# Kernel optimization log

Hardware: AMD Instinct MI355X
Metric: run time of the kernel (lower is better)

## Reference

```python
import jax, jax.numpy as jnp
import numpy as np

H = 12      # attention heads
BS = 64     # BigBird block size
NEG = -1e9  # additive mask value


def setup_inputs() -> dict:
    key = jax.random.key(0)
    ks = jax.random.split(key, 12)
    L, B, S, D, C = 13, 2, 512, 768, 16
    nb = (B * S) // BS  # 16 blocks
    w = lambda k, shp: jax.random.normal(k, shp, jnp.float32) * 0.02
    return {
        "hidden_states": jax.random.normal(ks[0], (L, B, S, D), jnp.float32),
        "attention_mask": jnp.ones((B, S), jnp.int32),
        # 3 random key-blocks per middle query block, drawn from non-global blocks
        "rand_blocks": jax.random.randint(ks[1], (nb - 2, 3), 1, nb - 1, jnp.int32),
        "Wq": w(ks[2], (D, D)), "bq": jnp.zeros((D,), jnp.float32),
        "Wk": w(ks[3], (D, D)), "bk": jnp.zeros((D,), jnp.float32),
        "Wv": w(ks[4], (D, D)), "bv": jnp.zeros((D,), jnp.float32),
        "Wo": w(ks[5], (D, D)), "bo": jnp.zeros((D,), jnp.float32),
        "Wd": w(ks[6], (D, D)), "bd": jnp.zeros((D,), jnp.float32),
        "ln_g": jnp.ones((D,), jnp.float32), "ln_b": jnp.zeros((D,), jnp.float32),
        "Wc": w(ks[7], (D, C)), "bc": jnp.zeros((C,), jnp.float32),
    }


def _forward(hidden_states, attention_mask, rand_blocks,
             Wq, bq, Wk, bk, Wv, bv, Wo, bo, Wd, bd, ln_g, ln_b, Wc, bc):
    L, B, S, D = hidden_states.shape
    T = B * S
    hd = D // H
    nb = T // BS
    scale = 1.0 / np.sqrt(hd).astype(np.float32)

    # tensor_split + cat glue == reshape to one row per layer
    h = hidden_states.reshape(L, T, D)           # [L,T,D]
    mask = attention_mask.reshape(T)             # [T]

    def proj(W, b):
        return (h @ W + b).reshape(L, T, H, hd).transpose(0, 2, 1, 3)  # [L,H,T,hd]

    q, k, v = proj(Wq, bq), proj(Wk, bk), proj(Wv, bv)
    qb = q.reshape(L, H, nb, BS, hd)
    kb = k.reshape(L, H, nb, BS, hd)
    vb = v.reshape(L, H, nb, BS, hd)
    maskb = mask.reshape(nb, BS)

    # ---- middle query blocks: global(first,last) + window(i-1,i,i+1) + 3 random ----
    nm = nb - 2
    mid = jnp.arange(1, nb - 1)
    glob = jnp.broadcast_to(jnp.array([0, nb - 1]), (nm, 2))
    win = jnp.stack([mid - 1, mid, mid + 1], axis=-1)          # [nm,3]
    idx = jnp.concatenate([glob, win, rand_blocks], axis=1)    # [nm,8]

    kg = kb[:, :, idx]                                         # [L,H,nm,8,BS,hd]
    vg = vb[:, :, idx].reshape(L, H, nm, 8 * BS, hd)
    mg = maskb[idx].reshape(nm, 8 * BS)                        # [nm,8*BS]

    qm = qb[:, :, 1:nb - 1]                                    # [L,H,nm,BS,hd]
    s = jnp.einsum('lhnqd,lhnkbd->lhnqkb', qm, kg).reshape(L, H, nm, BS, 8 * BS) * scale
    s = jnp.where(mg[None, None, :, None, :] > 0, s, NEG)
    a = jax.nn.softmax(s, axis=-1)
    ctx_mid = jnp.einsum('lhnqk,lhnkd->lhnqd', a, vg)          # [L,H,nm,BS,hd]

    # ---- global query blocks (first & last) attend to everything ----
    qg = qb[:, :, jnp.array([0, nb - 1])]                      # [L,H,2,BS,hd]
    sg = jnp.einsum('lhgqd,lhtd->lhgqt', qg, k) * scale
    sg = jnp.where(mask[None, None, None, None, :] > 0, sg, NEG)
    ag = jax.nn.softmax(sg, axis=-1)
    ctx_g = jnp.einsum('lhgqt,lhtd->lhgqd', ag, v)             # [L,H,2,BS,hd]

    ctx = jnp.concatenate([ctx_g[:, :, 0:1], ctx_mid, ctx_g[:, :, 1:2]], axis=2)
    ctx = ctx.transpose(0, 2, 3, 1, 4).reshape(L, T, D)        # [L,T,D]
    attn_out = ctx @ Wo + bo

    # BertSelfOutput: dense + LayerNorm (dropout = identity in eval)
    hs = attn_out @ Wd + bd
    mu = hs.mean(-1, keepdims=True)
    var = hs.var(-1, keepdims=True)
    hs = (hs - mu) / jnp.sqrt(var + 1e-12) * ln_g + ln_b

    out = hs[-1]                                               # last layer row, [T,D]
    batch_out = out.reshape(B, S, D)                           # un-flatten glue
    return batch_out @ Wc + bc                                 # [B,S,classes]


def reference(hidden_states, attention_mask, rand_blocks,
              Wq, bq, Wk, bk, Wv, bv, Wo, bo, Wd, bd, ln_g, ln_b, Wc, bc):
    return _forward(hidden_states, attention_mask, rand_blocks,
                    Wq, bq, Wk, bk, Wv, bv, Wo, bo, Wd, bd, ln_g, ln_b, Wc, bc)
```

## Files before the change

### kernel.cpp

```cpp
#include <hip/hip_runtime.h>
#include <hip/hip_bf16.h>
#include <math.h>

#define TT    1024
#define DD    768
#define NHEAD 12
#define HDIM  64
#define NBLK  16
#define NMID  14
#define NCOUT 16

typedef __attribute__((ext_vector_type(4))) float f32x4;
typedef __attribute__((ext_vector_type(8))) short bfrag;

#define MFMA(a, b, c) __builtin_amdgcn_mfma_f32_16x16x32_bf16(a, b, c, 0, 0, 0)

__device__ __forceinline__ bfrag ldg8(const ushort* p) { return *(const bfrag*)p; }
__device__ __forceinline__ ushort f2bf(float f) {
    __hip_bfloat16 h = __float2bfloat16(f);
    return *(ushort*)&h;
}

__global__ __launch_bounds__(256) void prep_k(
    const float* __restrict__ X,
    const float* __restrict__ Wq, const float* __restrict__ Wk,
    const float* __restrict__ Wv, const float* __restrict__ Wo,
    const float* __restrict__ Wd,
    ushort* __restrict__ xb,
    ushort* __restrict__ qT, ushort* __restrict__ kT, ushort* __restrict__ vT,
    ushort* __restrict__ oT, ushort* __restrict__ dT)
{
    __shared__ float t[32][33];
    int bx = blockIdx.x;
    if (bx < 768) {
        int i = bx * 256 + threadIdx.x;
        float4 f = ((const float4*)X)[i];
        ushort4 u;
        u.x = f2bf(f.x); u.y = f2bf(f.y); u.z = f2bf(f.z); u.w = f2bf(f.w);
        ((ushort4*)xb)[i] = u;
        return;
    }
    int bz = bx - 768;
    int z = bz / 576;
    int rem = bz % 576;
    int k0 = (rem / 24) * 32, n0 = (rem % 24) * 32;
    const float* W; ushort* O;
    if (z == 0)      { W = Wq; O = qT; }
    else if (z == 1) { W = Wk; O = kT; }
    else if (z == 2) { W = Wv; O = vT; }
    else if (z == 3) { W = Wo; O = oT; }
    else             { W = Wd; O = dT; }
    int tx = threadIdx.x & 31, ty = threadIdx.x >> 5;
    #pragma unroll
    for (int i = 0; i < 4; i++)
        t[ty + i * 8][tx] = W[(k0 + ty + i * 8) * DD + n0 + tx];
    __syncthreads();
    #pragma unroll
    for (int i = 0; i < 4; i++)
        O[(n0 + ty + i * 8) * DD + k0 + tx] = f2bf(t[tx][ty + i * 8]);
}

__global__ __launch_bounds__(256) void qkv_mfma_k(
    const ushort* __restrict__ xb,
    const ushort* __restrict__ wqT, const ushort* __restrict__ wkT,
    const ushort* __restrict__ wvT,
    const float* __restrict__ bq, const float* __restrict__ bk,
    const float* __restrict__ bv,
    ushort* __restrict__ qo, ushort* __restrict__ ko, ushort* __restrict__ vTo)
{
    int z = blockIdx.z;
    const ushort* BT = (z == 0) ? wqT : (z == 1) ? wkT : wvT;
    const float* bias = (z == 0) ? bq : (z == 1) ? bk : bv;

    __shared__ float mo[4][16][4][64];
    int lane = threadIdx.x & 63, w = threadIdx.x >> 6;
    int lr = lane & 15, lg = lane >> 4;
    int row0 = blockIdx.x * 64;
    int h = blockIdx.y;
    int col0 = h * 64;

    f32x4 acc[16];
    #pragma unroll
    for (int p = 0; p < 16; p++) acc[p] = (f32x4){0, 0, 0, 0};
    const ushort* ap = xb + (size_t)(row0 + lr) * DD + w * 192 + lg * 8;
    const ushort* bp = BT + (size_t)(col0 + lr) * DD + w * 192 + lg * 8;
    #pragma unroll
    for (int ks = 0; ks < 6; ks++) {
        bfrag a0 = ldg8(ap + ks * 32);
        bfrag a1 = ldg8(ap + (size_t)16 * DD + ks * 32);
        bfrag a2 = ldg8(ap + (size_t)32 * DD + ks * 32);
        bfrag a3 = ldg8(ap + (size_t)48 * DD + ks * 32);
        #pragma unroll
        for (int nt = 0; nt < 4; nt++) {
            bfrag b = ldg8(bp + (size_t)nt * 16 * DD + ks * 32);
            acc[nt]      = MFMA(a0, b, acc[nt]);
            acc[4 + nt]  = MFMA(a1, b, acc[4 + nt]);
            acc[8 + nt]  = MFMA(a2, b, acc[8 + nt]);
            acc[12 + nt] = MFMA(a3, b, acc[12 + nt]);
        }
    }
    #pragma unroll
    for (int p = 0; p < 16; p++)
        #pragma unroll
        for (int j = 0; j < 4; j++)
            mo[w][p][j][lane] = acc[p][j];
    __syncthreads();

    #pragma unroll
    for (int pi = 0; pi < 4; pi++) {
        int p = w + pi * 4;
        int m = p >> 2, nt = p & 3;
        #pragma unroll
        for (int j = 0; j < 4; j++) {
            float of = mo[0][p][j][lane] + mo[1][p][j][lane] +
                       mo[2][p][j][lane] + mo[3][p][j][lane];
            int r = row0 + m * 16 + lg * 4 + j;
            int cc = nt * 16 + lr;
            ushort u = f2bf(of + bias[col0 + cc]);
            if (z == 2)      vTo[(size_t)(h * 64 + cc) * TT + r] = u;
            else if (z == 0) qo[(size_t)(h * TT + r) * 64 + cc] = u;
            else             ko[(size_t)(h * TT + r) * 64 + cc] = u;
        }
    }
}

template <int OUTF32>
__global__ __launch_bounds__(256) void mm_mfma_k(
    const ushort* __restrict__ A, const ushort* __restrict__ BT,
    const float* __restrict__ bias, void* __restrict__ out)
{
    __shared__ float mo[4][8][4][64];
    int lane = threadIdx.x & 63, w = threadIdx.x >> 6;
    int lr = lane & 15, lg = lane >> 4;
    int row0 = blockIdx.x * 32;
    int col0 = blockIdx.y * 64;

    f32x4 acc[8];
    #pragma unroll
    for (int p = 0; p < 8; p++) acc[p] = (f32x4){0, 0, 0, 0};
    const ushort* a0p = A + (size_t)(row0 + lr) * DD + w * 192 + lg * 8;
    const ushort* a1p = a0p + (size_t)16 * DD;
    const ushort* bp  = BT + (size_t)(col0 + lr) * DD + w * 192 + lg * 8;
    #pragma unroll
    for (int ks = 0; ks < 6; ks++) {
        bfrag a0 = ldg8(a0p + ks * 32);
        bfrag a1 = ldg8(a1p + ks * 32);
        #pragma unroll
        for (int nt = 0; nt < 4; nt++) {
            bfrag b = ldg8(bp + (size_t)nt * 16 * DD + ks * 32);
            acc[nt]     = MFMA(a0, b, acc[nt]);
            acc[4 + nt] = MFMA(a1, b, acc[4 + nt]);
        }
    }
    #pragma unroll
    for (int p = 0; p < 8; p++)
        #pragma unroll
        for (int j = 0; j < 4; j++)
            mo[w][p][j][lane] = acc[p][j];
    __syncthreads();

    #pragma unroll
    for (int pi = 0; pi < 2; pi++) {
        int p = w + pi * 4;
        int m = p >> 2, nt = p & 3;
        #pragma unroll
        for (int j = 0; j < 4; j++) {
            float of = mo[0][p][j][lane] + mo[1][p][j][lane] +
                       mo[2][p][j][lane] + mo[3][p][j][lane];
            int r = row0 + m * 16 + lg * 4 + j;
            int c = col0 + nt * 16 + lr;
            float v = of + bias[c];
            if (OUTF32) ((float*)out)[(size_t)r * DD + c] = v;
            else        ((ushort*)out)[(size_t)r * DD + c] = f2bf(v);
        }
    }
}

__device__ __forceinline__ void attn_core2x2(
    const ushort* __restrict__ kbf, const ushort* __restrict__ vT,
    const int* __restrict__ mask, const int kblk[2], int h,
    bfrag aq0, bfrag aq1, bfrag aq2, bfrag aq3, ushort* __restrict__ Pw,
    f32x4 (&o0)[4], f32x4 (&o1)[4], float (&l0)[4], float (&l1)[4])
{
    int lane = threadIdx.x & 63, lr = lane & 15, lg = lane >> 4;
    #pragma unroll
    for (int kb = 0; kb < 2; kb++) {
        int bi = kblk[kb];
        #pragma unroll
        for (int kt = 0; kt < 4; kt++) {
            int key = bi * 64 + kt * 16 + lr;
            const ushort* krow = kbf + (size_t)(h * TT + key) * 64 + lg * 8;
            bfrag b0 = ldg8(krow);
            bfrag b1 = ldg8(krow + 32);
            f32x4 s0 = {0, 0, 0, 0}, s1 = {0, 0, 0, 0};
            s0 = MFMA(aq0, b0, s0); s0 = MFMA(aq1, b1, s0);
            s1 = MFMA(aq2, b0, s1); s1 = MFMA(aq3, b1, s1);
            int mk = mask[key];
            #pragma unroll
            for (int j = 0; j < 4; j++) {
                int row = lg * 4 + j;
                int base = (row * 128 + (kb * 4 + kt) * 16 + lr)
                           ^ ((row & 7) << 3);
                float p0 = (mk > 0) ? __expf(s0[j] * 0.125f) : 0.0f;
                l0[j] += p0;
                Pw[base] = f2bf(p0);
                float p1 = (mk > 0) ? __expf(s1[j] * 0.125f) : 0.0f;
                l1[j] += p1;
                Pw[2048 + base] = f2bf(p1);
            }
        }
    }
    #pragma unroll
    for (int ks = 0; ks < 4; ks++) {
        int bi = kblk[ks >> 1];
        int pidx = (lr * 128 + ks * 32 + lg * 8) ^ ((lr & 7) << 3);
        bfrag pa0 = *(const bfrag*)(Pw + pidx);
        bfrag pa1 = *(const bfrag*)(Pw + 2048 + pidx);
        #pragma unroll
        for (int dt = 0; dt < 4; dt++) {
            const ushort* vrow = vT + (size_t)(h * 64 + dt * 16 + lr) * TT
                               + bi * 64 + (ks & 1) * 32 + lg * 8;
            bfrag vv = ldg8(vrow);
            o0[dt] = MFMA(pa0, vv, o0[dt]);
            o1[dt] = MFMA(pa1, vv, o1[dt]);
        }
    }
}

__global__ __launch_bounds__(256, 3) void attn_k(
    const ushort* __restrict__ qbf, const ushort* __restrict__ kbf,
    const ushort* __restrict__ vT, const int* __restrict__ mask,
    const int* __restrict__ rnd, ushort* __restrict__ ctx)
{
    __shared__ __align__(16) ushort P[4][4096];
    __shared__ float mo[4][4][4][64];
    __shared__ float ml[4][16];
    int x = blockIdx.x, h = blockIdx.y;
    int w = threadIdx.x >> 6, lane = threadIdx.x & 63;
    int lr = lane & 15, lg = lane >> 4;

    int qtok0 = x * 32;
    int qb = x >> 1;
    const ushort* qrow = qbf + (size_t)(h * TT + qtok0 + lr) * 64 + lg * 8;
    bfrag aq0 = ldg8(qrow);
    bfrag aq1 = ldg8(qrow + 32);
    const ushort* qrow1 = qrow + (size_t)16 * 64;
    bfrag aq2 = ldg8(qrow1);
    bfrag aq3 = ldg8(qrow1 + 32);

    f32x4 zero = {0, 0, 0, 0};
    f32x4 o0[4] = {zero, zero, zero, zero};
    f32x4 o1[4] = {zero, zero, zero, zero};
    float l0[4] = {0.f, 0.f, 0.f, 0.f};
    float l1[4] = {0.f, 0.f, 0.f, 0.f};

    if (qb >= 1 && qb <= NMID) {
        int n = qb - 1;
        int b0, b1;
        if (w == 0)      { b0 = 0;              b1 = NBLK - 1;       }
        else if (w == 1) { b0 = n;              b1 = n + 1;          }
        else if (w == 2) { b0 = n + 2;          b1 = rnd[n * 3 + 0]; }
        else             { b0 = rnd[n * 3 + 1]; b1 = rnd[n * 3 + 2]; }
        int kblk[2] = { b0, b1 };
        attn_core2x2(kbf, vT, mask, kblk, h, aq0, aq1, aq2, aq3,
                     &P[w][0], o0, o1, l0, l1);
    } else {
        int kb0[2] = { w * 4, w * 4 + 1 };
        attn_core2x2(kbf, vT, mask, kb0, h, aq0, aq1, aq2, aq3,
                     &P[w][0], o0, o1, l0, l1);
        int kb1[2] = { w * 4 + 2, w * 4 + 3 };
        attn_core2x2(kbf, vT, mask, kb1, h, aq0, aq1, aq2, aq3,
                     &P[w][0], o0, o1, l0, l1);
    }

    #pragma unroll
    for (int j = 0; j < 4; j++) {
        float s0 = l0[j];
        s0 += __shfl_xor(s0, 1); s0 += __shfl_xor(s0, 2);
        s0 += __shfl_xor(s0, 4); s0 += __shfl_xor(s0, 8);
        l0[j] = s0;
        float s1 = l1[j];
        s1 += __shfl_xor(s1, 1); s1 += __shfl_xor(s1, 2);
        s1 += __shfl_xor(s1, 4); s1 += __shfl_xor(s1, 8);
        l1[j] = s1;
    }

    #pragma unroll
    for (int dt = 0; dt < 4; dt++)
        #pragma unroll
        for (int j = 0; j < 4; j++)
            mo[w][dt][j][lane] = o0[dt][j];
    if (lr == 0) {
        #pragma unroll
        for (int j = 0; j < 4; j++) ml[w][lg * 4 + j] = l0[j];
    }
    __syncthreads();
    #pragma unroll
    for (int j = 0; j < 4; j++) {
        int row = lg * 4 + j;
        float lt = 1.0f / (ml[0][row] + ml[1][row] + ml[2][row] + ml[3][row]);
        float of = mo[0][w][j][lane] + mo[1][w][j][lane] +
                   mo[2][w][j][lane] + mo[3][w][j][lane];
        ctx[(size_t)(qtok0 + row) * DD + h * 64 + w * 16 + lr] = f2bf(of * lt);
    }
    __syncthreads();

    #pragma unroll
    for (int dt = 0; dt < 4; dt++)
        #pragma unroll
        for (int j = 0; j < 4; j++)
            mo[w][dt][j][lane] = o1[dt][j];
    if (lr == 0) {
        #pragma unroll
        for (int j = 0; j < 4; j++) ml[w][lg * 4 + j] = l1[j];
    }
    __syncthreads();
    #pragma unroll
    for (int j = 0; j < 4; j++) {
        int row = lg * 4 + j;
        float lt = 1.0f / (ml[0][row] + ml[1][row] + ml[2][row] + ml[3][row]);
        float of = mo[0][w][j][lane] + mo[1][w][j][lane] +
                   mo[2][w][j][lane] + mo[3][w][j][lane];
        ctx[(size_t)(qtok0 + 16 + row) * DD + h * 64 + w * 16 + lr] =
            f2bf(of * lt);
    }
}

__global__ __launch_bounds__(256) void ln_out_k(
    const float* __restrict__ hs, const float* __restrict__ g,
    const float* __restrict__ b, const float* __restrict__ Wc,
    const float* __restrict__ bc, float* __restrict__ out)
{
    int tk = blockIdx.x;
    int tid = threadIdx.x;
    int wv = tid >> 6, ln_ = tid & 63;
    __shared__ float ws[2][4];
    __shared__ float hsn[768];

    float x0 = hs[tk * DD + tid];
    float x1 = hs[tk * DD + tid + 256];
    float x2 = hs[tk * DD + tid + 512];

    float s = x0 + x1 + x2;
    float q = x0 * x0 + x1 * x1 + x2 * x2;
    #pragma unroll
    for (int off = 1; off < 64; off <<= 1) {
        s += __shfl_xor(s, off);
        q += __shfl_xor(q, off);
    }
    if (ln_ == 0) { ws[0][wv] = s; ws[1][wv] = q; }
    __syncthreads();
    float S = ws[0][0] + ws[0][1] + ws[0][2] + ws[0][3];
    float Q = ws[1][0] + ws[1][1] + ws[1][2] + ws[1][3];
    float mean = S * (1.0f / 768.0f);
    float var = Q * (1.0f / 768.0f) - mean * mean;
    float rstd = rsqrtf(var + 1e-12f);

    hsn[tid]       = (x0 - mean) * rstd * g[tid]       + b[tid];
    hsn[tid + 256] = (x1 - mean) * rstd * g[tid + 256] + b[tid + 256];
    hsn[tid + 512] = (x2 - mean) * rstd * g[tid + 512] + b[tid + 512];
    __syncthreads();

    int c = tid >> 4, i = tid & 15;
    float acc = 0.0f;
    #pragma unroll 8
    for (int j = 0; j < 48; j++) {
        int kk = j * 16 + i;
        acc += hsn[kk] * Wc[kk * NCOUT + c];
    }
    acc += __shfl_xor(acc, 1); acc += __shfl_xor(acc, 2);
    acc += __shfl_xor(acc, 4); acc += __shfl_xor(acc, 8);
    if (i == 0) out[tk * NCOUT + c] = acc + bc[c];
}

extern "C" void kernel_launch(void* const* d_in, const int* in_sizes, int n_in,
                              void* d_out, int out_size, void* d_ws, size_t ws_size,
                              hipStream_t stream)
{
    const float* hidden = (const float*)d_in[0];
    const int*   mask   = (const int*)d_in[1];
    const int*   rnd    = (const int*)d_in[2];
    const float* Wq = (const float*)d_in[3];
    const float* bq = (const float*)d_in[4];
    const float* Wk = (const float*)d_in[5];
    const float* bk = (const float*)d_in[6];
    const float* Wv = (const float*)d_in[7];
    const float* bv = (const float*)d_in[8];
    const float* Wo = (const float*)d_in[9];
    const float* bo = (const float*)d_in[10];
    const float* Wd = (const float*)d_in[11];
    const float* bd = (const float*)d_in[12];
    const float* lng = (const float*)d_in[13];
    const float* lnb = (const float*)d_in[14];
    const float* Wc = (const float*)d_in[15];
    const float* bc = (const float*)d_in[16];
    float* out = (float*)d_out;

    int L = in_sizes[0] / (TT * DD);
    const float* X = hidden + (size_t)(L - 1) * TT * DD;

    const size_t TD  = (size_t)TT * DD;
    const size_t WSZ = (size_t)DD * DD;

    ushort* xb   = (ushort*)d_ws;
    ushort* wqT  = xb   + TD;
    ushort* wkT  = wqT  + WSZ;
    ushort* wvT  = wkT  + WSZ;
    ushort* woT  = wvT  + WSZ;
    ushort* wdT  = woT  + WSZ;
    ushort* qbf  = wdT  + WSZ;
    ushort* kbf  = qbf  + TD;
    ushort* vTb  = kbf  + TD;
    ushort* ctxb = vTb  + TD;
    ushort* attb = ctxb + TD;
    float*  hs   = (float*)(attb + TD);

    prep_k<<<768 + 2880, 256, 0, stream>>>(X, Wq, Wk, Wv, Wo, Wd,
                                           xb, wqT, wkT, wvT, woT, wdT);
    qkv_mfma_k<<<dim3(16, NHEAD, 3), 256, 0, stream>>>(xb, wqT, wkT, wvT,
                                                       bq, bk, bv, qbf, kbf, vTb);
    attn_k<<<dim3(32, NHEAD), 256, 0, stream>>>(qbf, kbf, vTb, mask, rnd, ctxb);
    mm_mfma_k<0><<<dim3(32, NHEAD), 256, 0, stream>>>(ctxb, woT, bo, attb);
    mm_mfma_k<1><<<dim3(32, NHEAD), 256, 0, stream>>>(attb, wdT, bd, hs);
    ln_out_k<<<TT, 256, 0, stream>>>(hs, lng, lnb, Wc, bc, out);
}
```

Measured before the change: 101.3 us.

## Split global-query attention across two blocks with a separate combine kernel

Global query blocks (first and last) attend to all 16 key blocks, so their workgroups did twice the work of middle ones and set the tail of the attention kernel. Each global sub-block now splits its keys into two halves handled by separate workgroups. These write unnormalized partial outputs and row sums to a workspace, and a small new kernel sums and normalizes them. This balances the load but adds a kernel launch, extra global traffic, and more workspace.

```diff
diff --git a/kernel.cpp b/kernel.cpp
--- a/kernel.cpp
+++ b/kernel.cpp
@@ -230,7 +230,8 @@
 __global__ __launch_bounds__(256, 3) void attn_k(
     const ushort* __restrict__ qbf, const ushort* __restrict__ kbf,
     const ushort* __restrict__ vT, const int* __restrict__ mask,
-    const int* __restrict__ rnd, ushort* __restrict__ ctx)
+    const int* __restrict__ rnd, ushort* __restrict__ ctx,
+    float* __restrict__ pacc, float* __restrict__ pl)
 {
     __shared__ __align__(16) ushort P[4][4096];
     __shared__ float mo[4][4][4][64];
@@ -239,8 +240,18 @@
     int w = threadIdx.x >> 6, lane = threadIdx.x & 63;
     int lr = lane & 15, lg = lane >> 4;
 
-    int qtok0 = x * 32;
-    int qb = x >> 1;
+    bool isMid = (x < 28);
+    int qb, sub, g = 0, z = 0;
+    if (isMid) { qb = 1 + (x >> 1); sub = x & 1; }
+    else {
+        int r = x - 28;
+        g = r >> 2;
+        sub = (r >> 1) & 1;
+        z = r & 1;
+        qb = g ? (NBLK - 1) : 0;
+    }
+    int qtok0 = qb * 64 + sub * 32;
+
     const ushort* qrow = qbf + (size_t)(h * TT + qtok0 + lr) * 64 + lg * 8;
     bfrag aq0 = ldg8(qrow);
     bfrag aq1 = ldg8(qrow + 32);
@@ -254,7 +265,7 @@
     float l0[4] = {0.f, 0.f, 0.f, 0.f};
     float l1[4] = {0.f, 0.f, 0.f, 0.f};
 
-    if (qb >= 1 && qb <= NMID) {
+    if (isMid) {
         int n = qb - 1;
         int b0, b1;
         if (w == 0)      { b0 = 0;              b1 = NBLK - 1;       }
@@ -265,11 +276,8 @@
         attn_core2x2(kbf, vT, mask, kblk, h, aq0, aq1, aq2, aq3,
                      &P[w][0], o0, o1, l0, l1);
     } else {
-        int kb0[2] = { w * 4, w * 4 + 1 };
-        attn_core2x2(kbf, vT, mask, kb0, h, aq0, aq1, aq2, aq3,
-                     &P[w][0], o0, o1, l0, l1);
-        int kb1[2] = { w * 4 + 2, w * 4 + 3 };
-        attn_core2x2(kbf, vT, mask, kb1, h, aq0, aq1, aq2, aq3,
+        int kblk[2] = { z * 8 + w * 2, z * 8 + w * 2 + 1 };
+        attn_core2x2(kbf, vT, mask, kblk, h, aq0, aq1, aq2, aq3,
                      &P[w][0], o0, o1, l0, l1);
     }
 
@@ -285,6 +293,9 @@
         l1[j] = s1;
     }
 
+    int slot = ((g * 2 + sub) * 2 + z) * NHEAD + h;
+    float* pb = pacc + (size_t)slot * 2048;
+
     #pragma unroll
     for (int dt = 0; dt < 4; dt++)
         #pragma unroll
@@ -298,10 +309,16 @@
     #pragma unroll
     for (int j = 0; j < 4; j++) {
         int row = lg * 4 + j;
-        float lt = 1.0f / (ml[0][row] + ml[1][row] + ml[2][row] + ml[3][row]);
+        float lsum = ml[0][row] + ml[1][row] + ml[2][row] + ml[3][row];
         float of = mo[0][w][j][lane] + mo[1][w][j][lane] +
                    mo[2][w][j][lane] + mo[3][w][j][lane];
-        ctx[(size_t)(qtok0 + row) * DD + h * 64 + w * 16 + lr] = f2bf(of * lt);
+        if (isMid) {
+            ctx[(size_t)(qtok0 + row) * DD + h * 64 + w * 16 + lr] =
+                f2bf(of / lsum);
+        } else {
+            pb[row * 64 + w * 16 + lr] = of;
+            if (w == 0 && lr == 0) pl[slot * 32 + row] = lsum;
+        }
     }
     __syncthreads();
 
@@ -318,11 +335,38 @@
     #pragma unroll
     for (int j = 0; j < 4; j++) {
         int row = lg * 4 + j;
-        float lt = 1.0f / (ml[0][row] + ml[1][row] + ml[2][row] + ml[3][row]);
+        float lsum = ml[0][row] + ml[1][row] + ml[2][row] + ml[3][row];
         float of = mo[0][w][j][lane] + mo[1][w][j][lane] +
                    mo[2][w][j][lane] + mo[3][w][j][lane];
-        ctx[(size_t)(qtok0 + 16 + row) * DD + h * 64 + w * 16 + lr] =
-            f2bf(of * lt);
+        if (isMid) {
+            ctx[(size_t)(qtok0 + 16 + row) * DD + h * 64 + w * 16 + lr] =
+                f2bf(of / lsum);
+        } else {
+            pb[(16 + row) * 64 + w * 16 + lr] = of;
+            if (w == 0 && lr == 0) pl[slot * 32 + 16 + row] = lsum;
+        }
+    }
+}
+
+__global__ __launch_bounds__(256) void glob_comb_k(
+    const float* __restrict__ pacc, const float* __restrict__ pl,
+    ushort* __restrict__ ctx)
+{
+    int t = blockIdx.x, h = blockIdx.y;
+    int g = t >> 1, sub = t & 1;
+    int qtok0 = (g ? (NBLK - 1) : 0) * 64 + sub * 32;
+    int slot0 = (t * 2 + 0) * NHEAD + h;
+    int slot1 = (t * 2 + 1) * NHEAD + h;
+    const float* p0 = pacc + (size_t)slot0 * 2048;
+    const float* p1 = pacc + (size_t)slot1 * 2048;
+    int tid = threadIdx.x;
+    #pragma unroll
+    for (int it = 0; it < 8; it++) {
+        int e = tid + it * 256;
+        int r = e >> 6, c = e & 63;
+        float l = pl[slot0 * 32 + r] + pl[slot1 * 32 + r];
+        float v = (p0[e] + p1[e]) / l;
+        ctx[(size_t)(qtok0 + r) * DD + h * 64 + c] = f2bf(v);
     }
 }
 
@@ -414,12 +458,16 @@
     ushort* ctxb = vTb  + TD;
     ushort* attb = ctxb + TD;
     float*  hs   = (float*)(attb + TD);
+    float*  pacc = hs + TD;
+    float*  pl   = pacc + (size_t)96 * 2048;
 
     prep_k<<<768 + 2880, 256, 0, stream>>>(X, Wq, Wk, Wv, Wo, Wd,
                                            xb, wqT, wkT, wvT, woT, wdT);
     qkv_mfma_k<<<dim3(16, NHEAD, 3), 256, 0, stream>>>(xb, wqT, wkT, wvT,
                                                        bq, bk, bv, qbf, kbf, vTb);
-    attn_k<<<dim3(32, NHEAD), 256, 0, stream>>>(qbf, kbf, vTb, mask, rnd, ctxb);
+    attn_k<<<dim3(36, NHEAD), 256, 0, stream>>>(qbf, kbf, vTb, mask, rnd,
+                                                ctxb, pacc, pl);
+    glob_comb_k<<<dim3(4, NHEAD), 256, 0, stream>>>(pacc, pl, ctxb);
     mm_mfma_k<0><<<dim3(32, NHEAD), 256, 0, stream>>>(ctxb, woT, bo, attb);
     mm_mfma_k<1><<<dim3(32, NHEAD), 256, 0, stream>>>(attb, wdT, bd, hs);
     ln_out_k<<<TT, 256, 0, stream>>>(hs, lng, lnb, Wc, bc, out);
```

After: 92.82 us, median of 3. 1.09x faster.
